# Kernel tuning notes

Measured on AMD Instinct MI355X. Metric: run time of the kernel, lower is better.

The kernel has to match this reference:

```python
import jax, jax.numpy as jnp
import numpy as np

L, E, H, FF = 6, 768, 4, 3072
D = E // H
SCALE = float(E) ** -0.5  # note: source scales by embedding_size**-0.5, not head_dim
EPS = 1e-5


def layernorm(x, scale, bias):
    mu = jnp.mean(x, axis=-1, keepdims=True)
    var = jnp.mean((x - mu) ** 2, axis=-1, keepdims=True)
    return (x - mu) * jax.lax.rsqrt(var + EPS) * scale + bias


def setup_inputs() -> dict:
    key = jax.random.key(0)
    ks = jax.random.split(key, 16)
    s = 0.02
    inp = {
        "hidden_states": jax.random.normal(ks[0], (8, 1024, E), dtype=jnp.float32),
        "ln1_scale": jnp.ones((L, E), jnp.float32),
        "ln1_bias": jnp.zeros((L, E), jnp.float32),
        "wq": jax.random.normal(ks[1], (L, E, E), jnp.float32) * s,
        "wk": jax.random.normal(ks[2], (L, E, E), jnp.float32) * s,
        "wv": jax.random.normal(ks[3], (L, E, E), jnp.float32) * s,
        "wo": jax.random.normal(ks[4], (L, E, E), jnp.float32) * s,
        "bo": jnp.zeros((L, E), jnp.float32),
        "ln2_scale": jnp.ones((L, E), jnp.float32),
        "ln2_bias": jnp.zeros((L, E), jnp.float32),
        "w1": jax.random.normal(ks[5], (L, FF, E), jnp.float32) * s,
        "b1": jnp.zeros((L, FF), jnp.float32),
        "w2": jax.random.normal(ks[6], (L, E, FF), jnp.float32) * s,
        "b2": jnp.zeros((L, E), jnp.float32),
    }
    return inp


def _encoder(x, ln1_scale, ln1_bias, wq, wk, wv, wo, bo, ln2_scale, ln2_bias, w1, b1, w2, b2):
    B, S, _ = x.shape
    for i in range(L):
        h = layernorm(x, ln1_scale[i], ln1_bias[i])
        # torch Linear: y = x @ W.T
        q = (h @ wq[i].T).reshape(B, H, S, D)  # non-standard head split (reshape, no transpose) per source
        k = (h @ wk[i].T).reshape(B, H, S, D)
        v = (h @ wv[i].T).reshape(B, H, S, D)
        scores = jnp.einsum("bhsd,bhtd->bhst", q, k) * SCALE  # full SxS materialized, as in source
        attn = jax.nn.softmax(scores, axis=-1)
        o = jnp.einsum("bhst,bhtd->bhsd", attn, v)
        o = o.transpose(0, 2, 1, 3).reshape(B, S, E)
        x = x + (o @ wo[i].T + bo[i])
        h = layernorm(x, ln2_scale[i], ln2_bias[i])
        h = jax.nn.gelu(h @ w1[i].T + b1[i], approximate=False)  # nn.GELU default = exact erf
        x = x + (h @ w2[i].T + b2[i])  # dropout is identity in eval
    return x


def reference(hidden_states, ln1_scale, ln1_bias, wq, wk, wv, wo, bo, ln2_scale, ln2_bias, w1, b1, w2, b2):
    return _encoder(hidden_states, ln1_scale, ln1_bias, wq, wk, wv, wo, bo, ln2_scale, ln2_bias, w1, b1, w2, b2)
```

## Files before the change

### kernel.cpp

```cpp
#include <hip/hip_runtime.h>
#include <math.h>

typedef __attribute__((ext_vector_type(8))) __bf16 bf16x8;
typedef __attribute__((ext_vector_type(4))) __bf16 bf16x4;
typedef __attribute__((ext_vector_type(2))) __bf16 bf16x2;
typedef __attribute__((ext_vector_type(4))) float f32x4;

#define MFMA_BF16 __builtin_amdgcn_mfma_f32_16x16x32_bf16

constexpr int LAY = 6, E = 768, HH = 4, DH = 192, FF = 3072, BB = 8, SS = 1024, MM = 8192;
constexpr float ATT_SCALE = 0.03608439182435161f;

__device__ __forceinline__ void gl2lds16(const void* g, void* l) {
    __builtin_amdgcn_global_load_lds(
        (const __attribute__((address_space(1))) void*)g,
        (__attribute__((address_space(3))) void*)l, 16, 0, 0);
}

struct Cast6 {
    const float* src[6];
    __bf16* dst[6];
    int cum4[7];
};

__global__ __launch_bounds__(256) void cast6_kernel(Cast6 c, int total4) {
    int stride = gridDim.x * 256;
    for (int i = blockIdx.x * 256 + threadIdx.x; i < total4; i += stride) {
        int rgn = 0;
#pragma unroll
        for (int k = 1; k < 6; ++k) rgn += (i >= c.cum4[k]) ? 1 : 0;
        int off = i - c.cum4[rgn];
        f32x4 v = ((const f32x4*)c.src[rgn])[off];
        bf16x4 o;
        o[0] = (__bf16)v[0]; o[1] = (__bf16)v[1]; o[2] = (__bf16)v[2]; o[3] = (__bf16)v[3];
        ((bf16x4*)c.dst[rgn])[off] = o;
    }
}

__global__ __launch_bounds__(256) void ln_kernel(const float* __restrict__ x,
                                                 const float* __restrict__ gamma,
                                                 const float* __restrict__ beta,
                                                 __bf16* __restrict__ out) {
    size_t row = blockIdx.x;
    const float* xr = x + row * E;
    int t = threadIdx.x;
    float v0 = xr[t], v1 = xr[t + 256], v2 = xr[t + 512];
    float s = v0 + v1 + v2;
    float q = v0 * v0 + v1 * v1 + v2 * v2;
#pragma unroll
    for (int m = 1; m < 64; m <<= 1) { s += __shfl_xor(s, m); q += __shfl_xor(q, m); }
    __shared__ float red[8];
    int w = t >> 6;
    if ((t & 63) == 0) { red[w] = s; red[4 + w] = q; }
    __syncthreads();
    s = red[0] + red[1] + red[2] + red[3];
    q = red[4] + red[5] + red[6] + red[7];
    float mu = s * (1.0f / E);
    float var = q * (1.0f / E) - mu * mu;
    float rs = rsqrtf(var + 1e-5f);
    __bf16* orow = out + row * E;
    orow[t]       = (__bf16)((v0 - mu) * rs * gamma[t]       + beta[t]);
    orow[t + 256] = (__bf16)((v1 - mu) * rs * gamma[t + 256] + beta[t + 256]);
    orow[t + 512] = (__bf16)((v2 - mu) * rs * gamma[t + 512] + beta[t + 512]);
}

template <int EPI>
__global__ __launch_bounds__(512, 2) void gemm256(
    const __bf16* __restrict__ A,
    const __bf16* __restrict__ B0, const __bf16* __restrict__ B1, const __bf16* __restrict__ B2,
    void* __restrict__ O0, void* __restrict__ O1, void* __restrict__ O2,
    const float* __restrict__ bias, int M, int N, int K) {
    __shared__ __bf16 lds[4 * 16384];
    int z = blockIdx.z;
    const __bf16* Bw = (z == 0) ? B0 : (z == 1) ? B1 : B2;
    void* Out = (z == 0) ? O0 : (z == 1) ? O1 : O2;
    int t = threadIdx.x;
    int w = t >> 6, lane = t & 63, b4 = lane >> 4, r = lane & 15;
    int gx = gridDim.x;
    int nwg = gx * gridDim.y;
    int bid = blockIdx.y * gx + blockIdx.x;
    int cpx = nwg >> 3;
    int swz = (bid & 7) * cpx + (bid >> 3);
    int bx = swz % gx, by = swz / gx;
    int mbase = by * 256, nbase = bx * 256;
    int wr = w >> 2, wc = w & 3;
    const f32x4 fz = {0.f, 0.f, 0.f, 0.f};
    f32x4 acc[8][4];
#pragma unroll
    for (int a1 = 0; a1 < 8; ++a1)
#pragma unroll
        for (int a2 = 0; a2 < 4; ++a2) acc[a1][a2] = fz;
    const __bf16* Ap = A + (size_t)mbase * K;
    const __bf16* Bp = Bw + (size_t)nbase * K;
    int nk = K >> 5;

    auto stageA = [&](int tt) {
        int slot = (tt & 3) * 16384;
        int k0 = tt * 32;
#pragma unroll
        for (int i = 0; i < 2; ++i) {
            int c = i * 512 + t;
            int row = c >> 2, cl = c & 3;
            int sc = cl ^ ((row >> 1) & 3);
            gl2lds16(Ap + (size_t)row * K + k0 + sc * 8,
                     (void*)(lds + slot + (i * 512 + w * 64) * 8));
        }
    };
    auto stageB = [&](int tt) {
        int slot = (tt & 3) * 16384 + 8192;
        int k0 = tt * 32;
#pragma unroll
        for (int i = 0; i < 2; ++i) {
            int c = i * 512 + t;
            int row = c >> 2, cl = c & 3;
            int sc = cl ^ ((row >> 1) & 3);
            gl2lds16(Bp + (size_t)row * K + k0 + sc * 8,
                     (void*)(lds + slot + (i * 512 + w * 64) * 8));
        }
    };

    int swch = (b4 ^ ((r >> 1) & 3)) * 8;
    int aoff = (wr * 128 + r) * 32 + swch;
    int boff = (wc * 64 + r) * 32 + swch;

    stageA(0); stageB(0); stageA(1); stageB(1); stageA(2); stageB(2);

    for (int tt = 0; tt < nk; ++tt) {
        if (tt < nk - 2)       asm volatile("s_waitcnt vmcnt(8)" ::: "memory");
        else if (tt == nk - 2) asm volatile("s_waitcnt vmcnt(4)" ::: "memory");
        else                   asm volatile("s_waitcnt vmcnt(0)" ::: "memory");
        __builtin_amdgcn_s_barrier();
        asm volatile("" ::: "memory");
        const __bf16* sa = lds + (tt & 3) * 16384;
        const __bf16* sb = sa + 8192;
        bool do_stage = (tt + 3) < nk;
        bf16x8 bfr[4], af[4];
#pragma unroll
        for (int ni = 0; ni < 4; ++ni) bfr[ni] = *(const bf16x8*)(sb + boff + ni * 512);
#pragma unroll
        for (int mi = 0; mi < 4; ++mi) af[mi] = *(const bf16x8*)(sa + aoff + mi * 512);
        if (do_stage) stageA(tt + 3);
        __builtin_amdgcn_s_setprio(1);
#pragma unroll
        for (int mi = 0; mi < 4; ++mi)
#pragma unroll
            for (int ni = 0; ni < 4; ++ni)
                acc[mi][ni] = MFMA_BF16(af[mi], bfr[ni], acc[mi][ni], 0, 0, 0);
        __builtin_amdgcn_s_setprio(0);
#pragma unroll
        for (int mi = 0; mi < 4; ++mi) af[mi] = *(const bf16x8*)(sa + aoff + (mi + 4) * 512);
        if (do_stage) stageB(tt + 3);
        __builtin_amdgcn_s_setprio(1);
#pragma unroll
        for (int mi = 0; mi < 4; ++mi)
#pragma unroll
            for (int ni = 0; ni < 4; ++ni)
                acc[mi + 4][ni] = MFMA_BF16(af[mi], bfr[ni], acc[mi + 4][ni], 0, 0, 0);
        __builtin_amdgcn_s_setprio(0);
    }

#pragma unroll
    for (int mi = 0; mi < 8; ++mi) {
#pragma unroll
        for (int ni = 0; ni < 4; ++ni) {
            int col = nbase + wc * 64 + ni * 16 + r;
#pragma unroll
            for (int j = 0; j < 4; ++j) {
                int rowi = mbase + wr * 128 + mi * 16 + b4 * 4 + j;
                float v = acc[mi][ni][j];
                if constexpr (EPI == 0) {
                    ((__bf16*)Out)[(size_t)rowi * N + col] = (__bf16)v;
                } else if constexpr (EPI == 1) {
                    v += bias[col];
                    float g = 0.5f * v * (1.0f + erff(v * 0.70710678118654752f));
                    ((__bf16*)Out)[(size_t)rowi * N + col] = (__bf16)g;
                } else {
                    float* X = (float*)Out;
                    X[(size_t)rowi * N + col] += v + bias[col];
                }
            }
        }
    }
}

__global__ __launch_bounds__(256) void vtrans_kernel(const __bf16* __restrict__ v,
                                                     __bf16* __restrict__ vt) {
    __shared__ __bf16 tile[64 * 72];
    int bh = blockIdx.y;
    int si = blockIdx.x / 3, di = blockIdx.x % 3;
    int t = threadIdx.x;
    const __bf16* src = v + (size_t)bh * (SS * DH) + (size_t)(si * 64) * DH + di * 64;
#pragma unroll
    for (int i = 0; i < 2; ++i) {
        int c = i * 256 + t;
        int sl = c >> 3, dc = c & 7;
        *(bf16x8*)(tile + sl * 72 + dc * 8) = *(const bf16x8*)(src + (size_t)sl * DH + dc * 8);
    }
    __syncthreads();
    __bf16* dst = vt + ((size_t)bh * DH + di * 64) * SS + si * 64;
#pragma unroll
    for (int i = 0; i < 2; ++i) {
        int c = i * 256 + t;
        int dl = c >> 3, sc = c & 7;
        bf16x8 o;
#pragma unroll
        for (int e = 0; e < 8; ++e) o[e] = tile[(sc * 8 + e) * 72 + dl];
        *(bf16x8*)(dst + (size_t)dl * SS + sc * 8) = o;
    }
}

__global__ __launch_bounds__(256) void attn_kernel(const __bf16* __restrict__ qp,
                                                   const __bf16* __restrict__ kp,
                                                   const __bf16* __restrict__ vtp,
                                                   __bf16* __restrict__ ao) {
    __shared__ __bf16 smK[64 * 192];
    __shared__ __bf16 smVt[192 * 64];
    __shared__ __bf16 smP[4 * 16 * 72];
    int qt = blockIdx.x, h = blockIdx.y, b = blockIdx.z;
    int t = threadIdx.x, w = t >> 6, lane = t & 63, b4 = lane >> 4, r = lane & 15;
    size_t base = (size_t)b * (SS * E) + (size_t)h * (SS * DH);
    const __bf16* Q = qp + base;
    const __bf16* Kg = kp + base;
    const __bf16* VtG = vtp + (size_t)(b * HH + h) * DH * SS;
    int q0 = qt * 64 + w * 16;
    bf16x8 qf[6];
#pragma unroll
    for (int ks = 0; ks < 6; ++ks)
        qf[ks] = *(const bf16x8*)(Q + (size_t)(q0 + r) * DH + ks * 32 + b4 * 8);
    const f32x4 fz = {0.f, 0.f, 0.f, 0.f};
    f32x4 oacc[12];
#pragma unroll
    for (int i = 0; i < 12; ++i) oacc[i] = fz;
    float m_r[4], l_r[4];
#pragma unroll
    for (int j = 0; j < 4; ++j) { m_r[j] = -1e30f; l_r[j] = 0.f; }
    __bf16* smPw = smP + w * (16 * 72);

    for (int kt = 0; kt < 16; ++kt) {
        const __bf16* Ks = Kg + (size_t)kt * 64 * DH;
#pragma unroll
        for (int i = 0; i < 6; ++i) {
            int c = i * 256 + t;
            int row = c / 24, cc = c - row * 24;
            int scc = (cc & 0x18) | ((cc ^ row) & 7);
            gl2lds16(Ks + (size_t)row * DH + scc * 8,
                     (void*)(smK + (i * 256 + w * 64) * 8));
        }
#pragma unroll
        for (int i = 0; i < 6; ++i) {
            int c = i * 256 + t;
            int row = c >> 3, cc = c & 7;
            int scc = cc ^ (row & 7);
            gl2lds16(VtG + (size_t)row * SS + kt * 64 + scc * 8,
                     (void*)(smVt + (i * 256 + w * 64) * 8));
        }
        __syncthreads();
        f32x4 sc[4];
#pragma unroll
        for (int nt = 0; nt < 4; ++nt) sc[nt] = fz;
#pragma unroll
        for (int ks = 0; ks < 6; ++ks) {
#pragma unroll
            for (int nt = 0; nt < 4; ++nt) {
                int cc = ks * 4 + b4;
                int ccs = (cc & 0x18) | ((cc ^ r) & 7);
                bf16x8 kf = *(const bf16x8*)(smK + (nt * 16 + r) * 192 + ccs * 8);
                sc[nt] = MFMA_BF16(qf[ks], kf, sc[nt], 0, 0, 0);
            }
        }
#pragma unroll
        for (int nt = 0; nt < 4; ++nt) sc[nt] *= ATT_SCALE;
        float alpha[4];
#pragma unroll
        for (int j = 0; j < 4; ++j) {
            float mx = fmaxf(fmaxf(sc[0][j], sc[1][j]), fmaxf(sc[2][j], sc[3][j]));
#pragma unroll
            for (int msk = 1; msk < 16; msk <<= 1) mx = fmaxf(mx, __shfl_xor(mx, msk));
            float mn = fmaxf(m_r[j], mx);
            alpha[j] = __expf(m_r[j] - mn);
            m_r[j] = mn;
            float p0 = __expf(sc[0][j] - mn);
            float p1 = __expf(sc[1][j] - mn);
            float p2 = __expf(sc[2][j] - mn);
            float p3 = __expf(sc[3][j] - mn);
            sc[0][j] = p0; sc[1][j] = p1; sc[2][j] = p2; sc[3][j] = p3;
            float ps = p0 + p1 + p2 + p3;
#pragma unroll
            for (int msk = 1; msk < 16; msk <<= 1) ps += __shfl_xor(ps, msk);
            l_r[j] = l_r[j] * alpha[j] + ps;
        }
        {
            f32x4 a4 = {alpha[0], alpha[1], alpha[2], alpha[3]};
#pragma unroll
            for (int i = 0; i < 12; ++i) oacc[i] *= a4;
        }
#pragma unroll
        for (int nt = 0; nt < 4; ++nt)
#pragma unroll
            for (int j = 0; j < 4; ++j)
                smPw[(b4 * 4 + j) * 72 + nt * 16 + r] = (__bf16)sc[nt][j];
        __asm__ volatile("s_waitcnt lgkmcnt(0)" ::: "memory");
#pragma unroll
        for (int kt2 = 0; kt2 < 2; ++kt2) {
            bf16x8 pa = *(const bf16x8*)(smPw + r * 72 + kt2 * 32 + b4 * 8);
#pragma unroll
            for (int nt = 0; nt < 12; ++nt) {
                int ccs = (kt2 * 4 + b4) ^ (r & 7);
                bf16x8 vf = *(const bf16x8*)(smVt + (nt * 16 + r) * 64 + ccs * 8);
                oacc[nt] = MFMA_BF16(pa, vf, oacc[nt], 0, 0, 0);
            }
        }
        __syncthreads();
    }
    float inv[4];
#pragma unroll
    for (int j = 0; j < 4; ++j) inv[j] = 1.0f / l_r[j];
    __bf16* obase = ao + (size_t)b * (SS * E);
#pragma unroll
    for (int nt = 0; nt < 12; ++nt)
#pragma unroll
        for (int j = 0; j < 4; ++j) {
            int srow = q0 + b4 * 4 + j;
            obase[(size_t)srow * E + h * DH + nt * 16 + r] = (__bf16)(oacc[nt][j] * inv[j]);
        }
}

extern "C" void kernel_launch(void* const* d_in, const int* in_sizes, int n_in,
                              void* d_out, int out_size, void* d_ws, size_t ws_size,
                              hipStream_t stream) {
    const float* hs   = (const float*)d_in[0];
    const float* ln1s = (const float*)d_in[1];
    const float* ln1b = (const float*)d_in[2];
    const float* wq   = (const float*)d_in[3];
    const float* wk   = (const float*)d_in[4];
    const float* wv   = (const float*)d_in[5];
    const float* wo   = (const float*)d_in[6];
    const float* bo   = (const float*)d_in[7];
    const float* ln2s = (const float*)d_in[8];
    const float* ln2b = (const float*)d_in[9];
    const float* w1   = (const float*)d_in[10];
    const float* b1   = (const float*)d_in[11];
    const float* w2   = (const float*)d_in[12];
    const float* b2   = (const float*)d_in[13];
    float* X = (float*)d_out;

    char* ws = (char*)d_ws;
    size_t off = 0;
    auto alloc = [&](size_t bytes) {
        char* p = ws + off;
        off += (bytes + 255) & ~(size_t)255;
        return p;
    };
    __bf16* wq_b = (__bf16*)alloc((size_t)E * E * 2);
    __bf16* wk_b = (__bf16*)alloc((size_t)E * E * 2);
    __bf16* wv_b = (__bf16*)alloc((size_t)E * E * 2);
    __bf16* wo_b = (__bf16*)alloc((size_t)E * E * 2);
    __bf16* w1_b = (__bf16*)alloc((size_t)FF * E * 2);
    __bf16* w2_b = (__bf16*)alloc((size_t)FF * E * 2);
    __bf16* h_b  = (__bf16*)alloc((size_t)MM * E * 2);
    char* U = alloc((size_t)MM * FF * 2);
    const size_t SLOT = (size_t)MM * E * 2;
    __bf16* q_b  = (__bf16*)U;
    __bf16* k_b  = (__bf16*)(U + SLOT);
    __bf16* v_b  = (__bf16*)(U + 2 * SLOT);
    __bf16* vt_b = (__bf16*)(U + 3 * SLOT);
    __bf16* a_b  = (__bf16*)(U + 2 * SLOT);
    __bf16* f_b  = (__bf16*)U;

    hipMemcpyAsync(d_out, hs, (size_t)MM * E * 4, hipMemcpyDeviceToDevice, stream);

    for (int i = 0; i < LAY; ++i) {
        Cast6 c;
        c.src[0] = wq + (size_t)i * E * E;  c.dst[0] = wq_b;
        c.src[1] = wk + (size_t)i * E * E;  c.dst[1] = wk_b;
        c.src[2] = wv + (size_t)i * E * E;  c.dst[2] = wv_b;
        c.src[3] = wo + (size_t)i * E * E;  c.dst[3] = wo_b;
        c.src[4] = w1 + (size_t)i * FF * E; c.dst[4] = w1_b;
        c.src[5] = w2 + (size_t)i * FF * E; c.dst[5] = w2_b;
        int n4[6] = {E * E / 4, E * E / 4, E * E / 4, E * E / 4, FF * E / 4, FF * E / 4};
        c.cum4[0] = 0;
        for (int k = 0; k < 6; ++k) c.cum4[k + 1] = c.cum4[k] + n4[k];
        int total4 = c.cum4[6];
        cast6_kernel<<<1024, 256, 0, stream>>>(c, total4);

        ln_kernel<<<MM, 256, 0, stream>>>(X, ln1s + (size_t)i * E, ln1b + (size_t)i * E, h_b);

        gemm256<0><<<dim3(E / 256, MM / 256, 3), 512, 0, stream>>>(
            h_b, wq_b, wk_b, wv_b, q_b, k_b, v_b, nullptr, MM, E, E);

        vtrans_kernel<<<dim3(48, 32), 256, 0, stream>>>(v_b, vt_b);

        attn_kernel<<<dim3(SS / 64, HH, BB), 256, 0, stream>>>(q_b, k_b, vt_b, a_b);

        gemm256<2><<<dim3(E / 256, MM / 256, 1), 512, 0, stream>>>(
            a_b, wo_b, wo_b, wo_b, X, X, X, bo + (size_t)i * E, MM, E, E);

        ln_kernel<<<MM, 256, 0, stream>>>(X, ln2s + (size_t)i * E, ln2b + (size_t)i * E, h_b);

        gemm256<1><<<dim3(FF / 256, MM / 256, 1), 512, 0, stream>>>(
            h_b, w1_b, w1_b, w1_b, f_b, f_b, f_b, b1 + (size_t)i * FF, MM, FF, E);

        gemm256<2><<<dim3(E / 256, MM / 256, 1), 512, 0, stream>>>(
            f_b, w2_b, w2_b, w2_b, X, X, X, b2 + (size_t)i * E, MM, E, FF);
    }
}
```

Baseline: 2.121 ms.

## Restructure GEMM main loop into 64-wide K tiles with ping-pong LDS and interleaved barriers

Replaces the 4-slot, 32-wide K ring buffer in the 256x256 GEMM with two 64-wide K buffers, each split into two 32-wide halves. Each loop iteration now runs four MFMA phases separated by workgroup barriers, and global-to-LDS loads for the next tiles are issued between those phases. The aim is a more regular, ping-pong style overlap of loads and MFMA work across the wavefronts. The cost is many more s_barrier calls per iteration and more fragile vmcnt accounting, which could stall the waves.

```diff
diff --git a/kernel.cpp b/kernel.cpp
--- a/kernel.cpp
+++ b/kernel.cpp
@@ -70,7 +70,7 @@
     const __bf16* __restrict__ B0, const __bf16* __restrict__ B1, const __bf16* __restrict__ B2,
     void* __restrict__ O0, void* __restrict__ O1, void* __restrict__ O2,
     const float* __restrict__ bias, int M, int N, int K) {
-    __shared__ __bf16 lds[4 * 16384];
+    __shared__ __bf16 lds[2 * 32768];
     int z = blockIdx.z;
     const __bf16* Bw = (z == 0) ? B0 : (z == 1) ? B1 : B2;
     void* Out = (z == 0) ? O0 : (z == 1) ? O1 : O2;
@@ -92,54 +92,44 @@
         for (int a2 = 0; a2 < 4; ++a2) acc[a1][a2] = fz;
     const __bf16* Ap = A + (size_t)mbase * K;
     const __bf16* Bp = Bw + (size_t)nbase * K;
-    int nk = K >> 5;
-
-    auto stageA = [&](int tt) {
-        int slot = (tt & 3) * 16384;
-        int k0 = tt * 32;
+    int nt = K >> 6;
+
+    auto stage = [&](const __bf16* P, int regionB, int tt, int h) {
+        int reg = (tt & 1) * 32768 + regionB * 16384 + h * 8192;
 #pragma unroll
         for (int i = 0; i < 2; ++i) {
             int c = i * 512 + t;
             int row = c >> 2, cl = c & 3;
             int sc = cl ^ ((row >> 1) & 3);
-            gl2lds16(Ap + (size_t)row * K + k0 + sc * 8,
-                     (void*)(lds + slot + (i * 512 + w * 64) * 8));
+            gl2lds16(P + (size_t)row * K + tt * 64 + h * 32 + sc * 8,
+                     (void*)(lds + reg + (i * 512 + w * 64) * 8));
         }
     };
-    auto stageB = [&](int tt) {
-        int slot = (tt & 3) * 16384 + 8192;
-        int k0 = tt * 32;
-#pragma unroll
-        for (int i = 0; i < 2; ++i) {
-            int c = i * 512 + t;
-            int row = c >> 2, cl = c & 3;
-            int sc = cl ^ ((row >> 1) & 3);
-            gl2lds16(Bp + (size_t)row * K + k0 + sc * 8,
-                     (void*)(lds + slot + (i * 512 + w * 64) * 8));
-        }
-    };
-
     int swch = (b4 ^ ((r >> 1) & 3)) * 8;
     int aoff = (wr * 128 + r) * 32 + swch;
-    int boff = (wc * 64 + r) * 32 + swch;
-
-    stageA(0); stageB(0); stageA(1); stageB(1); stageA(2); stageB(2);
-
-    for (int tt = 0; tt < nk; ++tt) {
-        if (tt < nk - 2)       asm volatile("s_waitcnt vmcnt(8)" ::: "memory");
-        else if (tt == nk - 2) asm volatile("s_waitcnt vmcnt(4)" ::: "memory");
-        else                   asm volatile("s_waitcnt vmcnt(0)" ::: "memory");
-        __builtin_amdgcn_s_barrier();
-        asm volatile("" ::: "memory");
-        const __bf16* sa = lds + (tt & 3) * 16384;
-        const __bf16* sb = sa + 8192;
-        bool do_stage = (tt + 3) < nk;
-        bf16x8 bfr[4], af[4];
-#pragma unroll
-        for (int ni = 0; ni < 4; ++ni) bfr[ni] = *(const bf16x8*)(sb + boff + ni * 512);
+    int boff = 16384 + (wc * 64 + r) * 32 + swch;
+
+    stage(Ap, 0, 0, 0); stage(Bp, 1, 0, 0); stage(Ap, 0, 0, 1); stage(Bp, 1, 0, 1);
+    if (nt > 1) {
+        stage(Ap, 0, 1, 0); stage(Bp, 1, 1, 0);
+        asm volatile("s_waitcnt vmcnt(4)" ::: "memory");
+    } else {
+        asm volatile("s_waitcnt vmcnt(0)" ::: "memory");
+    }
+    __builtin_amdgcn_s_barrier();
+
+    for (int tt = 0; tt < nt; ++tt) {
+        const __bf16* sa = lds + (tt & 1) * 32768;
+        bf16x8 af[4], bfr[4];
+        bool st1 = (tt + 1) < nt, st2 = (tt + 2) < nt;
+
+#pragma unroll
+        for (int ni = 0; ni < 4; ++ni) bfr[ni] = *(const bf16x8*)(sa + boff + ni * 512);
 #pragma unroll
         for (int mi = 0; mi < 4; ++mi) af[mi] = *(const bf16x8*)(sa + aoff + mi * 512);
-        if (do_stage) stageA(tt + 3);
+        if (st1) stage(Ap, 0, tt + 1, 1);
+        __builtin_amdgcn_s_barrier();
+        asm volatile("s_waitcnt lgkmcnt(0)" ::: "memory");
         __builtin_amdgcn_s_setprio(1);
 #pragma unroll
         for (int mi = 0; mi < 4; ++mi)
@@ -147,9 +137,13 @@
             for (int ni = 0; ni < 4; ++ni)
                 acc[mi][ni] = MFMA_BF16(af[mi], bfr[ni], acc[mi][ni], 0, 0, 0);
         __builtin_amdgcn_s_setprio(0);
+        __builtin_amdgcn_s_barrier();
+
 #pragma unroll
         for (int mi = 0; mi < 4; ++mi) af[mi] = *(const bf16x8*)(sa + aoff + (mi + 4) * 512);
-        if (do_stage) stageB(tt + 3);
+        if (st1) stage(Bp, 1, tt + 1, 1);
+        __builtin_amdgcn_s_barrier();
+        asm volatile("s_waitcnt lgkmcnt(0)" ::: "memory");
         __builtin_amdgcn_s_setprio(1);
 #pragma unroll
         for (int mi = 0; mi < 4; ++mi)
@@ -157,6 +151,39 @@
             for (int ni = 0; ni < 4; ++ni)
                 acc[mi + 4][ni] = MFMA_BF16(af[mi], bfr[ni], acc[mi + 4][ni], 0, 0, 0);
         __builtin_amdgcn_s_setprio(0);
+        __builtin_amdgcn_s_barrier();
+
+#pragma unroll
+        for (int ni = 0; ni < 4; ++ni) bfr[ni] = *(const bf16x8*)(sa + 8192 + boff + ni * 512);
+#pragma unroll
+        for (int mi = 0; mi < 4; ++mi) af[mi] = *(const bf16x8*)(sa + 8192 + aoff + mi * 512);
+        if (st2) stage(Ap, 0, tt + 2, 0);
+        __builtin_amdgcn_s_barrier();
+        asm volatile("s_waitcnt lgkmcnt(0)" ::: "memory");
+        __builtin_amdgcn_s_setprio(1);
+#pragma unroll
+        for (int mi = 0; mi < 4; ++mi)
+#pragma unroll
+            for (int ni = 0; ni < 4; ++ni)
+                acc[mi][ni] = MFMA_BF16(af[mi], bfr[ni], acc[mi][ni], 0, 0, 0);
+        __builtin_amdgcn_s_setprio(0);
+        __builtin_amdgcn_s_barrier();
+
+#pragma unroll
+        for (int mi = 0; mi < 4; ++mi) af[mi] = *(const bf16x8*)(sa + 8192 + aoff + (mi + 4) * 512);
+        if (st2) stage(Bp, 1, tt + 2, 0);
+        __builtin_amdgcn_s_barrier();
+        asm volatile("s_waitcnt lgkmcnt(0)" ::: "memory");
+        __builtin_amdgcn_s_setprio(1);
+#pragma unroll
+        for (int mi = 0; mi < 4; ++mi)
+#pragma unroll
+            for (int ni = 0; ni < 4; ++ni)
+                acc[mi + 4][ni] = MFMA_BF16(af[mi], bfr[ni], acc[mi + 4][ni], 0, 0, 0);
+        __builtin_amdgcn_s_setprio(0);
+        if (st2) asm volatile("s_waitcnt vmcnt(4)" ::: "memory");
+        else     asm volatile("s_waitcnt vmcnt(0)" ::: "memory");
+        __builtin_amdgcn_s_barrier();
     }
 
 #pragma unroll
```

New measurement: 2.236 ms. +5.4%, slower.
